# Optimization experiments

Measured on AMD Instinct MI355X. Metric: run time of the kernel, lower is better.

Reference implementation:

```python
import jax, jax.numpy as jnp
import numpy as np

B, S, H = 128, 1024, 256
NEG = 1e9

def setup_inputs() -> dict:
    key = jax.random.key(0)
    ks = jax.random.split(key, 11)
    sc = 0.05
    return {
        'ref': jax.random.normal(ks[0], (B, S, H), jnp.float32),
        'query': jax.random.normal(ks[1], (B, H), jnp.float32),
        'mask': jax.random.randint(ks[2], (B, S), 0, 2, jnp.int32),
        'wg': jax.random.normal(ks[3], (H, H), jnp.float32) * sc,
        'bg': jax.random.normal(ks[4], (H,), jnp.float32) * sc,
        'wqg': jax.random.normal(ks[5], (H, H), jnp.float32) * sc,
        'vg': jax.random.normal(ks[6], (H,), jnp.float32) * sc,
        'wp': jax.random.normal(ks[7], (H, H), jnp.float32) * sc,
        'bp': jax.random.normal(ks[8], (H,), jnp.float32) * sc,
        'wqp': jax.random.normal(ks[9], (H, H), jnp.float32) * sc,
        'vp': jax.random.normal(ks[10], (H,), jnp.float32) * sc,
    }

def reference(ref, query, mask, wg, bg, wqg, vg, wp, bp, wqp, vp):
    # Bahdanau additive pointer attention with glimpse, per PointerDecoder.pointer_net
    maskf = mask.astype(ref.dtype)
    # glimpse attention
    enc_g = jnp.einsum('bsd,hd->bsh', ref, wg) + bg            # conv1d kernel=1
    q_g = jnp.einsum('bd,hd->bh', query, wqg)                   # w_q_g (no bias)
    scores_g = jnp.einsum('bsh,h->bs', jnp.tanh(enc_g + q_g[:, None, :]), vg)
    att_g = jax.nn.softmax(scores_g - maskf * NEG, axis=-1)     # [B,S]
    glimpse = jnp.einsum('bs,bsd->bd', att_g, ref) + query      # [B,H]
    # pointer scores
    enc_p = jnp.einsum('bsd,hd->bsh', ref, wp) + bp
    q_p = jnp.einsum('bd,hd->bh', glimpse, wqp)
    scores_p = jnp.einsum('bsh,h->bs', jnp.tanh(enc_p + q_p[:, None, :]), vp)
    masked_scores = scores_p - maskf * NEG                      # [B,S]
    return masked_scores
```

## Files before the change

kernel.cpp:

```cpp
#include <hip/hip_runtime.h>

#define Bb 128
#define Ss 1024
#define Hh 256
#define NEGF 1e9f

typedef short bf16x8 __attribute__((ext_vector_type(8)));
typedef float f32x4 __attribute__((ext_vector_type(4)));

__device__ __forceinline__ short f2bf(float f) {
    union { float f; unsigned u; } c; c.f = f;
    return (short)((c.u + 0x8000u) >> 16);
}

__device__ __forceinline__ float bfhi2f(unsigned u) {
    union { unsigned u; float f; } c; c.u = u & 0xFFFF0000u; return c.f;
}
__device__ __forceinline__ float bflo2f(unsigned u) {
    union { unsigned u; float f; } c; c.u = u << 16; return c.f;
}

__device__ __forceinline__ bf16x8 ld_bf8_f32(const float* p) {
    const float4* p4 = (const float4*)p;
    float4 a = p4[0], b = p4[1];
    bf16x8 r;
    r[0] = f2bf(a.x); r[1] = f2bf(a.y); r[2] = f2bf(a.z); r[3] = f2bf(a.w);
    r[4] = f2bf(b.x); r[5] = f2bf(b.y); r[6] = f2bf(b.z); r[7] = f2bf(b.w);
    return r;
}

__device__ __forceinline__ float fast_tanh(float x) {
    float cl = fminf(fmaxf(x, -10.f), 10.f);
    float e = __expf(2.f * cl);
    return (e - 1.f) * __builtin_amdgcn_rcpf(e + 1.f);
}

__device__ __forceinline__ void stage16(const short* g, short* l) {
    __builtin_amdgcn_global_load_lds((const __attribute__((address_space(1))) void*)g,
                                     (__attribute__((address_space(3))) void*)l, 16, 0, 0);
}

__global__ __launch_bounds__(256) void prep_kernel(const float* __restrict__ wg,
                                                   const float* __restrict__ wp,
                                                   const float* __restrict__ query,
                                                   const float* __restrict__ wqg,
                                                   const float* __restrict__ bg,
                                                   short* __restrict__ wgb,
                                                   short* __restrict__ wpb,
                                                   float* __restrict__ qbias_g) {
    int blk = blockIdx.x, t = threadIdx.x;
    if (blk < 256) {
        int i = blk * 256 + t;
        wgb[i] = f2bf(wg[i]);
        wpb[i] = f2bf(wp[i]);
    } else {
        int b = blk - 256;
        const float4* qr = (const float4*)(query + b * Hh);
        const float4* wr = (const float4*)(wqg + t * Hh);
        float acc = 0.f;
#pragma unroll 8
        for (int i = 0; i < Hh / 4; ++i) {
            float4 q4 = qr[i], w4 = wr[i];
            acc += q4.x * w4.x + q4.y * w4.y + q4.z * w4.z + q4.w * w4.w;
        }
        qbias_g[b * Hh + t] = acc + bg[t];
    }
}

template <int MASKED, int LOADF32>
__global__ __launch_bounds__(1024) void scores_mfma(const float* __restrict__ reff,
                                                    const short* __restrict__ refb_in,
                                                    short* __restrict__ refb_out,
                                                    const short* __restrict__ Wbf,
                                                    const float* __restrict__ qbias,
                                                    const float* __restrict__ vvec,
                                                    const int* __restrict__ mask,
                                                    float* __restrict__ out) {
    __shared__ __align__(16) short Wlds[65536];
    const int t = threadIdx.x;
    const int wave = t >> 6;
    const int lane = t & 63;
    const int nl = lane & 15;
    const int quad = lane >> 4;

    {
        const short* g = Wbf + (wave * 16 + nl) * Hh + quad * 8;
        short* l = &Wlds[wave * 4096];
#pragma unroll
        for (int kb = 0; kb < 8; ++kb)
            stage16(g + kb * 32, l + kb * 512);
    }

    const int tile = blockIdx.x * 16 + wave;
    const int b = tile >> 5;
    const int srow0 = (tile & 31) * 32;
    const float* qb_row = qbias + b * Hh;

    __syncthreads();

#pragma unroll
    for (int rt = 0; rt < 2; ++rt) {
        const size_t rowoff = ((size_t)b * Ss + srow0 + rt * 16 + nl) * Hh;

        bf16x8 afrag[8];
        if (LOADF32) {
            const float* rp = reff + rowoff + quad * 8;
#pragma unroll
            for (int kb = 0; kb < 8; ++kb)
                afrag[kb] = ld_bf8_f32(rp + kb * 32);
            short* dst = refb_out + rowoff + quad * 8;
#pragma unroll
            for (int kb = 0; kb < 8; ++kb)
                *(bf16x8*)(dst + kb * 32) = afrag[kb];
        } else {
            const short* rp = refb_in + rowoff + quad * 8;
#pragma unroll
            for (int kb = 0; kb < 8; ++kb)
                afrag[kb] = *(const bf16x8*)(rp + kb * 32);
        }

        float sc[4] = {0.f, 0.f, 0.f, 0.f};
#pragma unroll
        for (int nc = 0; nc < 16; ++nc) {
            const int n = nc * 16 + nl;
            const float qb = qb_row[n];
            const float vv = vvec[n];
            const short* wl = &Wlds[nc * 4096 + lane * 8];
            f32x4 c = {0.f, 0.f, 0.f, 0.f};
#pragma unroll
            for (int kb = 0; kb < 8; ++kb)
                c = __builtin_amdgcn_mfma_f32_16x16x32_bf16(
                    afrag[kb], *(const bf16x8*)(wl + kb * 512), c, 0, 0, 0);
#pragma unroll
            for (int r = 0; r < 4; ++r)
                sc[r] += fast_tanh(c[r] + qb) * vv;
        }

#pragma unroll
        for (int r = 0; r < 4; ++r) {
            float v = sc[r];
            v += __shfl_xor(v, 1, 64);
            v += __shfl_xor(v, 2, 64);
            v += __shfl_xor(v, 4, 64);
            v += __shfl_xor(v, 8, 64);
            sc[r] = v;
        }

        if (nl == 0) {
#pragma unroll
            for (int r = 0; r < 4; ++r) {
                int m = srow0 + rt * 16 + quad * 4 + r;
                float v = sc[r];
                if (MASKED) v -= (float)mask[b * Ss + m] * NEGF;
                out[(size_t)b * Ss + m] = v;
            }
        }
    }
}

__global__ __launch_bounds__(1024) void softmax_kernel(const float* __restrict__ scores,
                                                       const int* __restrict__ mask,
                                                       float* __restrict__ att) {
    int b = blockIdx.x, t = threadIdx.x;
    __shared__ float red[16];
    int idx = b * Ss + t;
    float x = scores[idx] - (float)mask[idx] * NEGF;

    float m = x;
#pragma unroll
    for (int o = 1; o < 64; o <<= 1) m = fmaxf(m, __shfl_xor(m, o, 64));
    if ((t & 63) == 0) red[t >> 6] = m;
    __syncthreads();
    float M = red[0];
#pragma unroll
    for (int j = 1; j < 16; ++j) M = fmaxf(M, red[j]);
    __syncthreads();

    float e = __expf(x - M);
    float s = e;
#pragma unroll
    for (int o = 1; o < 64; o <<= 1) s += __shfl_xor(s, o, 64);
    if ((t & 63) == 0) red[t >> 6] = s;
    __syncthreads();
    float S = 0.f;
#pragma unroll
    for (int j = 0; j < 16; ++j) S += red[j];

    att[idx] = e * __builtin_amdgcn_rcpf(S);
}

__global__ __launch_bounds__(256) void glimpse_part(const unsigned* __restrict__ refb,
                                                    const float* __restrict__ att,
                                                    float* __restrict__ gpart) {
    int b = blockIdx.x, q = blockIdx.y, t = threadIdx.x;
    const int c = t & 31;
    const int rg = t >> 5;
    __shared__ float part[8][Hh];
    const unsigned* base = refb + ((size_t)(b * Ss + q * 128)) * (Hh / 2);
    const float* ap = att + b * Ss + q * 128;

    float acc[8] = {0.f, 0.f, 0.f, 0.f, 0.f, 0.f, 0.f, 0.f};
#pragma unroll 4
    for (int it = 0; it < 16; ++it) {
        int row = it * 8 + rg;
        float a = ap[row];
        uint4 v = *(const uint4*)(base + (size_t)row * (Hh / 2) + c * 4);
        acc[0] += a * bflo2f(v.x); acc[1] += a * bfhi2f(v.x);
        acc[2] += a * bflo2f(v.y); acc[3] += a * bfhi2f(v.y);
        acc[4] += a * bflo2f(v.z); acc[5] += a * bfhi2f(v.z);
        acc[6] += a * bflo2f(v.w); acc[7] += a * bfhi2f(v.w);
    }
#pragma unroll
    for (int j = 0; j < 8; ++j) part[rg][c * 8 + j] = acc[j];
    __syncthreads();
    float s = 0.f;
#pragma unroll
    for (int g = 0; g < 8; ++g) s += part[g][t];
    gpart[(size_t)(b * 8 + q) * Hh + t] = s;
}

__global__ __launch_bounds__(256) void qbias_p_kernel(const float* __restrict__ gpart,
                                                      const float* __restrict__ query,
                                                      const float* __restrict__ wqp,
                                                      const float* __restrict__ bp,
                                                      float* __restrict__ out) {
    int b = blockIdx.x, t = threadIdx.x;
    __shared__ __align__(16) float gl[Hh];
    float g = query[b * Hh + t];
#pragma unroll
    for (int q = 0; q < 8; ++q) g += gpart[(b * 8 + q) * Hh + t];
    gl[t] = g;
    __syncthreads();
    const float4* wr = (const float4*)(wqp + t * Hh);
    const float4* gp = (const float4*)gl;
    float acc = 0.f;
#pragma unroll 8
    for (int i = 0; i < Hh / 4; ++i) {
        float4 w4 = wr[i];
        float4 g4 = gp[i];
        acc += w4.x * g4.x + w4.y * g4.y + w4.z * g4.z + w4.w * g4.w;
    }
    out[b * Hh + t] = acc + bp[t];
}

extern "C" void kernel_launch(void* const* d_in, const int* in_sizes, int n_in,
                              void* d_out, int out_size, void* d_ws, size_t ws_size,
                              hipStream_t stream) {
    const float* ref   = (const float*)d_in[0];
    const float* query = (const float*)d_in[1];
    const int*   mask  = (const int*)d_in[2];
    const float* wg    = (const float*)d_in[3];
    const float* bg    = (const float*)d_in[4];
    const float* wqg   = (const float*)d_in[5];
    const float* vg    = (const float*)d_in[6];
    const float* wp    = (const float*)d_in[7];
    const float* bp    = (const float*)d_in[8];
    const float* wqp   = (const float*)d_in[9];
    const float* vp    = (const float*)d_in[10];
    float* out = (float*)d_out;

    char* ws = (char*)d_ws;
    short* ref_bf   = (short*)(ws + 0);
    size_t off = (size_t)Bb * Ss * Hh * 2;
    short* wg_bf    = (short*)(ws + off);               off += 131072;
    short* wp_bf    = (short*)(ws + off);               off += 131072;
    float* qbias_g  = (float*)(ws + off);               off += 131072;
    float* qbias_p  = (float*)(ws + off);               off += 131072;
    float* scores_g = (float*)(ws + off);               off += 524288;
    float* att      = (float*)(ws + off);               off += 524288;
    float* gpart    = (float*)(ws + off);

    prep_kernel<<<384, 256, 0, stream>>>(wg, wp, query, wqg, bg, wg_bf, wp_bf, qbias_g);
    scores_mfma<0, 1><<<256, 1024, 0, stream>>>(
        ref, nullptr, ref_bf, wg_bf, qbias_g, vg, nullptr, scores_g);
    softmax_kernel<<<Bb, Ss, 0, stream>>>(scores_g, mask, att);
    glimpse_part<<<dim3(Bb, 8), 256, 0, stream>>>((const unsigned*)ref_bf, att, gpart);
    qbias_p_kernel<<<Bb, Hh, 0, stream>>>(gpart, query, wqp, bp, qbias_p);
    scores_mfma<1, 0><<<256, 1024, 0, stream>>>(
        nullptr, ref_bf, nullptr, wp_bf, qbias_p, vp, mask, out);
}
```

Before: 321.6 us.

## Keep weight fragments in registers and move ref bf16 conversion into prep kernel

The scores kernel is restructured so each wave holds a 32-column slice of the weight matrix in registers and streams 256 ref rows through it. Partial scores across waves are reduced in shared memory at the end, replacing the old layout where each wave held a row tile and read all 256 weight columns from LDS. The fp32-to-bf16 conversion of ref moves out of the first scores kernel into the prep kernel as extra blocks. The aim is to remove LDS weight traffic and raise occupancy with 512-thread blocks. The cost is that the A fragments are now loaded per 16-row tile with less reuse across the N dimension, and ref goes through an extra global round trip in bf16.

```diff
diff --git a/kernel.cpp b/kernel.cpp
--- a/kernel.cpp
+++ b/kernel.cpp
@@ -20,24 +20,10 @@
     union { unsigned u; float f; } c; c.u = u << 16; return c.f;
 }
 
-__device__ __forceinline__ bf16x8 ld_bf8_f32(const float* p) {
-    const float4* p4 = (const float4*)p;
-    float4 a = p4[0], b = p4[1];
-    bf16x8 r;
-    r[0] = f2bf(a.x); r[1] = f2bf(a.y); r[2] = f2bf(a.z); r[3] = f2bf(a.w);
-    r[4] = f2bf(b.x); r[5] = f2bf(b.y); r[6] = f2bf(b.z); r[7] = f2bf(b.w);
-    return r;
-}
-
 __device__ __forceinline__ float fast_tanh(float x) {
     float cl = fminf(fmaxf(x, -10.f), 10.f);
     float e = __expf(2.f * cl);
     return (e - 1.f) * __builtin_amdgcn_rcpf(e + 1.f);
-}
-
-__device__ __forceinline__ void stage16(const short* g, short* l) {
-    __builtin_amdgcn_global_load_lds((const __attribute__((address_space(1))) void*)g,
-                                     (__attribute__((address_space(3))) void*)l, 16, 0, 0);
 }
 
 __global__ __launch_bounds__(256) void prep_kernel(const float* __restrict__ wg,
@@ -45,15 +31,17 @@
                                                    const float* __restrict__ query,
                                                    const float* __restrict__ wqg,
                                                    const float* __restrict__ bg,
+                                                   const float* __restrict__ ref,
                                                    short* __restrict__ wgb,
                                                    short* __restrict__ wpb,
-                                                   float* __restrict__ qbias_g) {
+                                                   float* __restrict__ qbias_g,
+                                                   short* __restrict__ refb) {
     int blk = blockIdx.x, t = threadIdx.x;
     if (blk < 256) {
         int i = blk * 256 + t;
         wgb[i] = f2bf(wg[i]);
         wpb[i] = f2bf(wp[i]);
-    } else {
+    } else if (blk < 384) {
         int b = blk - 256;
         const float4* qr = (const float4*)(query + b * Hh);
         const float4* wr = (const float4*)(wqg + t * Hh);
@@ -64,97 +52,81 @@
             acc += q4.x * w4.x + q4.y * w4.y + q4.z * w4.z + q4.w * w4.w;
         }
         qbias_g[b * Hh + t] = acc + bg[t];
-    }
-}
-
-template <int MASKED, int LOADF32>
-__global__ __launch_bounds__(1024) void scores_mfma(const float* __restrict__ reff,
-                                                    const short* __restrict__ refb_in,
-                                                    short* __restrict__ refb_out,
-                                                    const short* __restrict__ Wbf,
-                                                    const float* __restrict__ qbias,
-                                                    const float* __restrict__ vvec,
-                                                    const int* __restrict__ mask,
-                                                    float* __restrict__ out) {
-    __shared__ __align__(16) short Wlds[65536];
+    } else {
+        size_t i = (size_t)(blk - 384) * 2048 + (size_t)t * 8;
+        const float4* p4 = (const float4*)(ref + i);
+        float4 a = p4[0], b4 = p4[1];
+        bf16x8 r;
+        r[0] = f2bf(a.x);  r[1] = f2bf(a.y);  r[2] = f2bf(a.z);  r[3] = f2bf(a.w);
+        r[4] = f2bf(b4.x); r[5] = f2bf(b4.y); r[6] = f2bf(b4.z); r[7] = f2bf(b4.w);
+        *(bf16x8*)(refb + i) = r;
+    }
+}
+
+template <int MASKED>
+__global__ __launch_bounds__(512, 4) void scores_mfma(const short* __restrict__ refb,
+                                                      const short* __restrict__ Wbf,
+                                                      const float* __restrict__ qbias,
+                                                      const float* __restrict__ vvec,
+                                                      const int* __restrict__ mask,
+                                                      float* __restrict__ out) {
+    __shared__ float partial[8][256];
     const int t = threadIdx.x;
-    const int wave = t >> 6;
+    const int w = t >> 6;
     const int lane = t & 63;
     const int nl = lane & 15;
     const int quad = lane >> 4;
-
-    {
-        const short* g = Wbf + (wave * 16 + nl) * Hh + quad * 8;
-        short* l = &Wlds[wave * 4096];
+    const int b = blockIdx.x >> 2;
+    const int row0 = (blockIdx.x & 3) * 256;
+
+    bf16x8 bfrag[2][8];
+#pragma unroll
+    for (int nc = 0; nc < 2; ++nc) {
+        const short* wp = Wbf + (w * 32 + nc * 16 + nl) * Hh + quad * 8;
 #pragma unroll
         for (int kb = 0; kb < 8; ++kb)
-            stage16(g + kb * 32, l + kb * 512);
-    }
-
-    const int tile = blockIdx.x * 16 + wave;
-    const int b = tile >> 5;
-    const int srow0 = (tile & 31) * 32;
-    const float* qb_row = qbias + b * Hh;
-
-    __syncthreads();
-
-#pragma unroll
-    for (int rt = 0; rt < 2; ++rt) {
-        const size_t rowoff = ((size_t)b * Ss + srow0 + rt * 16 + nl) * Hh;
-
+            bfrag[nc][kb] = *(const bf16x8*)(wp + kb * 32);
+    }
+    const float qb0 = qbias[b * Hh + w * 32 + nl];
+    const float qb1 = qbias[b * Hh + w * 32 + 16 + nl];
+    const float vv0 = vvec[w * 32 + nl];
+    const float vv1 = vvec[w * 32 + 16 + nl];
+
+    const short* abase = refb + ((size_t)b * Ss + row0 + nl) * Hh + quad * 8;
+
+#pragma unroll 1
+    for (int tt = 0; tt < 16; ++tt) {
+        const short* rp = abase + (size_t)tt * 16 * Hh;
         bf16x8 afrag[8];
-        if (LOADF32) {
-            const float* rp = reff + rowoff + quad * 8;
-#pragma unroll
-            for (int kb = 0; kb < 8; ++kb)
-                afrag[kb] = ld_bf8_f32(rp + kb * 32);
-            short* dst = refb_out + rowoff + quad * 8;
-#pragma unroll
-            for (int kb = 0; kb < 8; ++kb)
-                *(bf16x8*)(dst + kb * 32) = afrag[kb];
-        } else {
-            const short* rp = refb_in + rowoff + quad * 8;
-#pragma unroll
-            for (int kb = 0; kb < 8; ++kb)
-                afrag[kb] = *(const bf16x8*)(rp + kb * 32);
+#pragma unroll
+        for (int kb = 0; kb < 8; ++kb)
+            afrag[kb] = *(const bf16x8*)(rp + kb * 32);
+
+        f32x4 c0 = {0.f, 0.f, 0.f, 0.f};
+        f32x4 c1 = {0.f, 0.f, 0.f, 0.f};
+#pragma unroll
+        for (int kb = 0; kb < 8; ++kb) {
+            c0 = __builtin_amdgcn_mfma_f32_16x16x32_bf16(afrag[kb], bfrag[0][kb], c0, 0, 0, 0);
+            c1 = __builtin_amdgcn_mfma_f32_16x16x32_bf16(afrag[kb], bfrag[1][kb], c1, 0, 0, 0);
         }
-
-        float sc[4] = {0.f, 0.f, 0.f, 0.f};
-#pragma unroll
-        for (int nc = 0; nc < 16; ++nc) {
-            const int n = nc * 16 + nl;
-            const float qb = qb_row[n];
-            const float vv = vvec[n];
-            const short* wl = &Wlds[nc * 4096 + lane * 8];
-            f32x4 c = {0.f, 0.f, 0.f, 0.f};
-#pragma unroll
-            for (int kb = 0; kb < 8; ++kb)
-                c = __builtin_amdgcn_mfma_f32_16x16x32_bf16(
-                    afrag[kb], *(const bf16x8*)(wl + kb * 512), c, 0, 0, 0);
-#pragma unroll
-            for (int r = 0; r < 4; ++r)
-                sc[r] += fast_tanh(c[r] + qb) * vv;
+#pragma unroll
+        for (int r = 0; r < 4; ++r) {
+            float s = fast_tanh(c0[r] + qb0) * vv0 + fast_tanh(c1[r] + qb1) * vv1;
+            s += __shfl_xor(s, 1, 64);
+            s += __shfl_xor(s, 2, 64);
+            s += __shfl_xor(s, 4, 64);
+            s += __shfl_xor(s, 8, 64);
+            if (nl == 0) partial[w][tt * 16 + quad * 4 + r] = s;
         }
-
-#pragma unroll
-        for (int r = 0; r < 4; ++r) {
-            float v = sc[r];
-            v += __shfl_xor(v, 1, 64);
-            v += __shfl_xor(v, 2, 64);
-            v += __shfl_xor(v, 4, 64);
-            v += __shfl_xor(v, 8, 64);
-            sc[r] = v;
-        }
-
-        if (nl == 0) {
-#pragma unroll
-            for (int r = 0; r < 4; ++r) {
-                int m = srow0 + rt * 16 + quad * 4 + r;
-                float v = sc[r];
-                if (MASKED) v -= (float)mask[b * Ss + m] * NEGF;
-                out[(size_t)b * Ss + m] = v;
-            }
-        }
+    }
+
+    __syncthreads();
+    if (t < 256) {
+        float s = 0.f;
+#pragma unroll
+        for (int g = 0; g < 8; ++g) s += partial[g][t];
+        if (MASKED) s -= (float)mask[b * Ss + row0 + t] * NEGF;
+        out[(size_t)b * Ss + row0 + t] = s;
     }
 }
 
@@ -270,12 +242,11 @@
     float* att      = (float*)(ws + off);               off += 524288;
     float* gpart    = (float*)(ws + off);
 
-    prep_kernel<<<384, 256, 0, stream>>>(wg, wp, query, wqg, bg, wg_bf, wp_bf, qbias_g);
-    scores_mfma<0, 1><<<256, 1024, 0, stream>>>(
-        ref, nullptr, ref_bf, wg_bf, qbias_g, vg, nullptr, scores_g);
+    prep_kernel<<<16768, 256, 0, stream>>>(wg, wp, query, wqg, bg, ref,
+                                           wg_bf, wp_bf, qbias_g, ref_bf);
+    scores_mfma<0><<<512, 512, 0, stream>>>(ref_bf, wg_bf, qbias_g, vg, nullptr, scores_g);
     softmax_kernel<<<Bb, Ss, 0, stream>>>(scores_g, mask, att);
     glimpse_part<<<dim3(Bb, 8), 256, 0, stream>>>((const unsigned*)ref_bf, att, gpart);
     qbias_p_kernel<<<Bb, Hh, 0, stream>>>(gpart, query, wqp, bp, qbias_p);
-    scores_mfma<1, 0><<<256, 1024, 0, stream>>>(
-        nullptr, ref_bf, nullptr, wp_bf, qbias_p, vp, mask, out);
-}
+    scores_mfma<1><<<512, 512, 0, stream>>>(ref_bf, wp_bf, qbias_p, vp, mask, out);
+}
```

New measurement: 368.1 us. 1.14x slower.

## Register-block four A tiles per wave and reuse LDS B fragments across them

Applied to the files above, without the earlier changes.

The scores kernel now runs 512-thread blocks (8 waves), each wave owning 64 rows held as four 16-row A tiles in registers. Each W chunk's B fragments are read from LDS once and reused across all four tiles, cutting LDS traffic per MFMA. All ref loads are issued up front before the barrier, so global latency overlaps the W staging. The cost is heavy register pressure (128 VGPRs for A fragments alone) and fewer waves per CU, which may limit latency hiding.

```diff
diff --git a/kernel.cpp b/kernel.cpp
--- a/kernel.cpp
+++ b/kernel.cpp
@@ -68,94 +68,97 @@
 }
 
 template <int MASKED, int LOADF32>
-__global__ __launch_bounds__(1024) void scores_mfma(const float* __restrict__ reff,
-                                                    const short* __restrict__ refb_in,
-                                                    short* __restrict__ refb_out,
-                                                    const short* __restrict__ Wbf,
-                                                    const float* __restrict__ qbias,
-                                                    const float* __restrict__ vvec,
-                                                    const int* __restrict__ mask,
-                                                    float* __restrict__ out) {
+__global__ __launch_bounds__(512, 1) void scores_mfma(const float* __restrict__ reff,
+                                                      const short* __restrict__ refb_in,
+                                                      short* __restrict__ refb_out,
+                                                      const short* __restrict__ Wbf,
+                                                      const float* __restrict__ qbias,
+                                                      const float* __restrict__ vvec,
+                                                      const int* __restrict__ mask,
+                                                      float* __restrict__ out) {
     __shared__ __align__(16) short Wlds[65536];
     const int t = threadIdx.x;
-    const int wave = t >> 6;
+    const int w = t >> 6;
     const int lane = t & 63;
     const int nl = lane & 15;
     const int quad = lane >> 4;
-
-    {
-        const short* g = Wbf + (wave * 16 + nl) * Hh + quad * 8;
-        short* l = &Wlds[wave * 4096];
+    const int b = blockIdx.x >> 1;
+    const int row0 = (blockIdx.x & 1) * 512 + w * 64;
+
+#pragma unroll
+    for (int h = 0; h < 2; ++h) {
+        const int nc = w * 2 + h;
+        const short* g = Wbf + (nc * 16 + nl) * Hh + quad * 8;
+        short* l = &Wlds[nc * 4096];
 #pragma unroll
         for (int kb = 0; kb < 8; ++kb)
             stage16(g + kb * 32, l + kb * 512);
     }
 
-    const int tile = blockIdx.x * 16 + wave;
-    const int b = tile >> 5;
-    const int srow0 = (tile & 31) * 32;
+    const size_t arow = (size_t)b * Ss + row0 + nl;
+    bf16x8 afrag[4][8];
+    if (LOADF32) {
+#pragma unroll
+        for (int tile = 0; tile < 4; ++tile) {
+            const float* rp = reff + (arow + tile * 16) * Hh + quad * 8;
+            short* dst = refb_out + (arow + tile * 16) * Hh + quad * 8;
+#pragma unroll
+            for (int kb = 0; kb < 8; ++kb) {
+                afrag[tile][kb] = ld_bf8_f32(rp + kb * 32);
+                *(bf16x8*)(dst + kb * 32) = afrag[tile][kb];
+            }
+        }
+    } else {
+#pragma unroll
+        for (int tile = 0; tile < 4; ++tile) {
+            const short* rp = refb_in + (arow + tile * 16) * Hh + quad * 8;
+#pragma unroll
+            for (int kb = 0; kb < 8; ++kb)
+                afrag[tile][kb] = *(const bf16x8*)(rp + kb * 32);
+        }
+    }
+
+    __syncthreads();
+
     const float* qb_row = qbias + b * Hh;
-
-    __syncthreads();
-
-#pragma unroll
-    for (int rt = 0; rt < 2; ++rt) {
-        const size_t rowoff = ((size_t)b * Ss + srow0 + rt * 16 + nl) * Hh;
-
-        bf16x8 afrag[8];
-        if (LOADF32) {
-            const float* rp = reff + rowoff + quad * 8;
+    float sc[4][4] = {{0.f, 0.f, 0.f, 0.f}, {0.f, 0.f, 0.f, 0.f},
+                      {0.f, 0.f, 0.f, 0.f}, {0.f, 0.f, 0.f, 0.f}};
+
+#pragma unroll 1
+    for (int nc = 0; nc < 16; ++nc) {
+        const float qb = qb_row[nc * 16 + nl];
+        const float vv = vvec[nc * 16 + nl];
+        bf16x8 bfrag[8];
+#pragma unroll
+        for (int kb = 0; kb < 8; ++kb)
+            bfrag[kb] = *(const bf16x8*)&Wlds[nc * 4096 + kb * 512 + lane * 8];
+#pragma unroll
+        for (int tile = 0; tile < 4; ++tile) {
+            f32x4 c = {0.f, 0.f, 0.f, 0.f};
 #pragma unroll
             for (int kb = 0; kb < 8; ++kb)
-                afrag[kb] = ld_bf8_f32(rp + kb * 32);
-            short* dst = refb_out + rowoff + quad * 8;
-#pragma unroll
-            for (int kb = 0; kb < 8; ++kb)
-                *(bf16x8*)(dst + kb * 32) = afrag[kb];
-        } else {
-            const short* rp = refb_in + rowoff + quad * 8;
-#pragma unroll
-            for (int kb = 0; kb < 8; ++kb)
-                afrag[kb] = *(const bf16x8*)(rp + kb * 32);
-        }
-
-        float sc[4] = {0.f, 0.f, 0.f, 0.f};
-#pragma unroll
-        for (int nc = 0; nc < 16; ++nc) {
-            const int n = nc * 16 + nl;
-            const float qb = qb_row[n];
-            const float vv = vvec[n];
-            const short* wl = &Wlds[nc * 4096 + lane * 8];
-            f32x4 c = {0.f, 0.f, 0.f, 0.f};
-#pragma unroll
-            for (int kb = 0; kb < 8; ++kb)
-                c = __builtin_amdgcn_mfma_f32_16x16x32_bf16(
-                    afrag[kb], *(const bf16x8*)(wl + kb * 512), c, 0, 0, 0);
+                c = __builtin_amdgcn_mfma_f32_16x16x32_bf16(afrag[tile][kb], bfrag[kb], c, 0, 0, 0);
 #pragma unroll
             for (int r = 0; r < 4; ++r)
-                sc[r] += fast_tanh(c[r] + qb) * vv;
-        }
-
+                sc[tile][r] += fast_tanh(c[r] + qb) * vv;
+        }
+    }
+
+#pragma unroll
+    for (int tile = 0; tile < 4; ++tile)
 #pragma unroll
         for (int r = 0; r < 4; ++r) {
-            float v = sc[r];
+            float v = sc[tile][r];
             v += __shfl_xor(v, 1, 64);
             v += __shfl_xor(v, 2, 64);
             v += __shfl_xor(v, 4, 64);
             v += __shfl_xor(v, 8, 64);
-            sc[r] = v;
-        }
-
-        if (nl == 0) {
-#pragma unroll
-            for (int r = 0; r < 4; ++r) {
-                int m = srow0 + rt * 16 + quad * 4 + r;
-                float v = sc[r];
+            if (nl == 0) {
+                int m = row0 + tile * 16 + quad * 4 + r;
                 if (MASKED) v -= (float)mask[b * Ss + m] * NEGF;
                 out[(size_t)b * Ss + m] = v;
             }
         }
-    }
 }
 
 __global__ __launch_bounds__(1024) void softmax_kernel(const float* __restrict__ scores,
@@ -271,11 +274,11 @@
     float* gpart    = (float*)(ws + off);
 
     prep_kernel<<<384, 256, 0, stream>>>(wg, wp, query, wqg, bg, wg_bf, wp_bf, qbias_g);
-    scores_mfma<0, 1><<<256, 1024, 0, stream>>>(
+    scores_mfma<0, 1><<<256, 512, 0, stream>>>(
         ref, nullptr, ref_bf, wg_bf, qbias_g, vg, nullptr, scores_g);
     softmax_kernel<<<Bb, Ss, 0, stream>>>(scores_g, mask, att);
     glimpse_part<<<dim3(Bb, 8), 256, 0, stream>>>((const unsigned*)ref_bf, att, gpart);
     qbias_p_kernel<<<Bb, Hh, 0, stream>>>(gpart, query, wqp, bp, qbias_p);
-    scores_mfma<1, 0><<<256, 1024, 0, stream>>>(
+    scores_mfma<1, 0><<<256, 512, 0, stream>>>(
         nullptr, ref_bf, nullptr, wp_bf, qbias_p, vp, mask, out);
 }
```

Result: faster. 307.7 us (-4.3%).

## Drop LDS weight staging, read weights from global per wave with smaller blocks

Applied to the files above, without the earlier changes.

The scores kernel no longer stages the full 128KB bf16 weight matrix into LDS per 1024-thread block. Each 256-thread block's waves now handle one 16-row tile and stream the weight fragments straight from global/L2, two N-tiles per step. This removes the 128KB LDS footprint that capped occupancy at one block per CU and the barrier before compute. The f32-to-bf16 conversion now uses a packed hardware convert instruction. In exchange, weight traffic through L2 rises since every wave re-reads all of W, and per-wave reuse drops from 32 rows to 16.

```diff
diff --git a/kernel.cpp b/kernel.cpp
--- a/kernel.cpp
+++ b/kernel.cpp
@@ -20,12 +20,9 @@
     union { unsigned u; float f; } c; c.u = u << 16; return c.f;
 }
 
-__device__ __forceinline__ bf16x8 ld_bf8_f32(const float* p) {
-    const float4* p4 = (const float4*)p;
-    float4 a = p4[0], b = p4[1];
-    bf16x8 r;
-    r[0] = f2bf(a.x); r[1] = f2bf(a.y); r[2] = f2bf(a.z); r[3] = f2bf(a.w);
-    r[4] = f2bf(b.x); r[5] = f2bf(b.y); r[6] = f2bf(b.z); r[7] = f2bf(b.w);
+__device__ __forceinline__ unsigned cvt_pk_bf16(float a, float b) {
+    unsigned r;
+    asm("v_cvt_pk_bf16_f32 %0, %1, %2" : "=v"(r) : "v"(a), "v"(b));
     return r;
 }
 
@@ -33,11 +30,6 @@
     float cl = fminf(fmaxf(x, -10.f), 10.f);
     float e = __expf(2.f * cl);
     return (e - 1.f) * __builtin_amdgcn_rcpf(e + 1.f);
-}
-
-__device__ __forceinline__ void stage16(const short* g, short* l) {
-    __builtin_amdgcn_global_load_lds((const __attribute__((address_space(1))) void*)g,
-                                     (__attribute__((address_space(3))) void*)l, 16, 0, 0);
 }
 
 __global__ __launch_bounds__(256) void prep_kernel(const float* __restrict__ wg,
@@ -68,92 +60,86 @@
 }
 
 template <int MASKED, int LOADF32>
-__global__ __launch_bounds__(1024) void scores_mfma(const float* __restrict__ reff,
-                                                    const short* __restrict__ refb_in,
-                                                    short* __restrict__ refb_out,
-                                                    const short* __restrict__ Wbf,
-                                                    const float* __restrict__ qbias,
-                                                    const float* __restrict__ vvec,
-                                                    const int* __restrict__ mask,
-                                                    float* __restrict__ out) {
-    __shared__ __align__(16) short Wlds[65536];
-    const int t = threadIdx.x;
-    const int wave = t >> 6;
-    const int lane = t & 63;
+__global__ __launch_bounds__(256) void scores_mfma(const float* __restrict__ reff,
+                                                   const short* __restrict__ refb_in,
+                                                   short* __restrict__ refb_out,
+                                                   const short* __restrict__ Wbf,
+                                                   const float* __restrict__ qbias,
+                                                   const float* __restrict__ vvec,
+                                                   const int* __restrict__ mask,
+                                                   float* __restrict__ out) {
+    const int T = blockIdx.x * 4 + (threadIdx.x >> 6);
+    const int lane = threadIdx.x & 63;
     const int nl = lane & 15;
     const int quad = lane >> 4;
-
-    {
-        const short* g = Wbf + (wave * 16 + nl) * Hh + quad * 8;
-        short* l = &Wlds[wave * 4096];
+    const int b = T >> 6;
+    const int row0 = (T & 63) * 16;
+    const size_t abase = ((size_t)b * Ss + row0 + nl) * Hh + quad * 8;
+
+    bf16x8 afrag[8];
+    if (LOADF32) {
+        float4 f[16];
+        const float* rp = reff + abase;
+#pragma unroll
+        for (int kb = 0; kb < 8; ++kb) {
+            f[2 * kb]     = *(const float4*)(rp + kb * 32);
+            f[2 * kb + 1] = *(const float4*)(rp + kb * 32 + 4);
+        }
+#pragma unroll
+        for (int kb = 0; kb < 8; ++kb) {
+            union { unsigned u[4]; bf16x8 v; } cv;
+            cv.u[0] = cvt_pk_bf16(f[2 * kb].x,     f[2 * kb].y);
+            cv.u[1] = cvt_pk_bf16(f[2 * kb].z,     f[2 * kb].w);
+            cv.u[2] = cvt_pk_bf16(f[2 * kb + 1].x, f[2 * kb + 1].y);
+            cv.u[3] = cvt_pk_bf16(f[2 * kb + 1].z, f[2 * kb + 1].w);
+            afrag[kb] = cv.v;
+            *(bf16x8*)(refb_out + abase + kb * 32) = cv.v;
+        }
+    } else {
+        const short* rp = refb_in + abase;
 #pragma unroll
         for (int kb = 0; kb < 8; ++kb)
-            stage16(g + kb * 32, l + kb * 512);
-    }
-
-    const int tile = blockIdx.x * 16 + wave;
-    const int b = tile >> 5;
-    const int srow0 = (tile & 31) * 32;
-    const float* qb_row = qbias + b * Hh;
-
-    __syncthreads();
-
-#pragma unroll
-    for (int rt = 0; rt < 2; ++rt) {
-        const size_t rowoff = ((size_t)b * Ss + srow0 + rt * 16 + nl) * Hh;
-
-        bf16x8 afrag[8];
-        if (LOADF32) {
-            const float* rp = reff + rowoff + quad * 8;
-#pragma unroll
-            for (int kb = 0; kb < 8; ++kb)
-                afrag[kb] = ld_bf8_f32(rp + kb * 32);
-            short* dst = refb_out + rowoff + quad * 8;
-#pragma unroll
-            for (int kb = 0; kb < 8; ++kb)
-                *(bf16x8*)(dst + kb * 32) = afrag[kb];
-        } else {
-            const short* rp = refb_in + rowoff + quad * 8;
-#pragma unroll
-            for (int kb = 0; kb < 8; ++kb)
-                afrag[kb] = *(const bf16x8*)(rp + kb * 32);
-        }
-
-        float sc[4] = {0.f, 0.f, 0.f, 0.f};
-#pragma unroll
-        for (int nc = 0; nc < 16; ++nc) {
-            const int n = nc * 16 + nl;
-            const float qb = qb_row[n];
-            const float vv = vvec[n];
-            const short* wl = &Wlds[nc * 4096 + lane * 8];
-            f32x4 c = {0.f, 0.f, 0.f, 0.f};
-#pragma unroll
-            for (int kb = 0; kb < 8; ++kb)
-                c = __builtin_amdgcn_mfma_f32_16x16x32_bf16(
-                    afrag[kb], *(const bf16x8*)(wl + kb * 512), c, 0, 0, 0);
-#pragma unroll
-            for (int r = 0; r < 4; ++r)
-                sc[r] += fast_tanh(c[r] + qb) * vv;
-        }
-
-#pragma unroll
-        for (int r = 0; r < 4; ++r) {
-            float v = sc[r];
-            v += __shfl_xor(v, 1, 64);
-            v += __shfl_xor(v, 2, 64);
-            v += __shfl_xor(v, 4, 64);
-            v += __shfl_xor(v, 8, 64);
-            sc[r] = v;
-        }
-
+            afrag[kb] = *(const bf16x8*)(rp + kb * 32);
+    }
+
+    const float* qb = qbias + b * Hh;
+    float rs[4] = {0.f, 0.f, 0.f, 0.f};
+
+#pragma unroll 1
+    for (int s = 0; s < 8; ++s) {
+        const short* w0 = Wbf + (s * 32 + nl) * Hh + quad * 8;
+        const short* w1 = w0 + 16 * Hh;
+        bf16x8 bf0[8], bf1[8];
+#pragma unroll
+        for (int kb = 0; kb < 8; ++kb) {
+            bf0[kb] = *(const bf16x8*)(w0 + kb * 32);
+            bf1[kb] = *(const bf16x8*)(w1 + kb * 32);
+        }
+        f32x4 c0 = {0.f, 0.f, 0.f, 0.f};
+        f32x4 c1 = {0.f, 0.f, 0.f, 0.f};
+#pragma unroll
+        for (int kb = 0; kb < 8; ++kb) {
+            c0 = __builtin_amdgcn_mfma_f32_16x16x32_bf16(afrag[kb], bf0[kb], c0, 0, 0, 0);
+            c1 = __builtin_amdgcn_mfma_f32_16x16x32_bf16(afrag[kb], bf1[kb], c1, 0, 0, 0);
+        }
+        const float q0 = qb[s * 32 + nl],       q1 = qb[s * 32 + 16 + nl];
+        const float v0 = vvec[s * 32 + nl],     v1 = vvec[s * 32 + 16 + nl];
+#pragma unroll
+        for (int r = 0; r < 4; ++r)
+            rs[r] += fast_tanh(c0[r] + q0) * v0 + fast_tanh(c1[r] + q1) * v1;
+    }
+
+#pragma unroll
+    for (int r = 0; r < 4; ++r) {
+        float v = rs[r];
+        v += __shfl_xor(v, 1, 64);
+        v += __shfl_xor(v, 2, 64);
+        v += __shfl_xor(v, 4, 64);
+        v += __shfl_xor(v, 8, 64);
         if (nl == 0) {
-#pragma unroll
-            for (int r = 0; r < 4; ++r) {
-                int m = srow0 + rt * 16 + quad * 4 + r;
-                float v = sc[r];
-                if (MASKED) v -= (float)mask[b * Ss + m] * NEGF;
-                out[(size_t)b * Ss + m] = v;
-            }
+            int m = row0 + quad * 4 + r;
+            if (MASKED) v -= (float)mask[b * Ss + m] * NEGF;
+            out[(size_t)b * Ss + m] = v;
         }
     }
 }
@@ -271,11 +257,11 @@
     float* gpart    = (float*)(ws + off);
 
     prep_kernel<<<384, 256, 0, stream>>>(wg, wp, query, wqg, bg, wg_bf, wp_bf, qbias_g);
-    scores_mfma<0, 1><<<256, 1024, 0, stream>>>(
+    scores_mfma<0, 1><<<2048, 256, 0, stream>>>(
         ref, nullptr, ref_bf, wg_bf, qbias_g, vg, nullptr, scores_g);
     softmax_kernel<<<Bb, Ss, 0, stream>>>(scores_g, mask, att);
     glimpse_part<<<dim3(Bb, 8), 256, 0, stream>>>((const unsigned*)ref_bf, att, gpart);
     qbias_p_kernel<<<Bb, Hh, 0, stream>>>(gpart, query, wqp, bp, qbias_p);
-    scores_mfma<1, 0><<<256, 1024, 0, stream>>>(
+    scores_mfma<1, 0><<<2048, 256, 0, stream>>>(
         nullptr, ref_bf, nullptr, wp_bf, qbias_p, vp, mask, out);
 }
```

Measured after the change: 485.3 us. 1.51x slower.
